# Optimization experiments

Measured on AMD Instinct MI355X. Metric: run time of the kernel, lower is better.

The kernel has to match this reference:

```python
import jax, jax.numpy as jnp
import numpy as np

B, T, H = 2048, 512, 128  # batch, seq_len, lstm_dim
IN = 1  # LSTMCell input dim = 1 + c_dim (condition=False)


def setup_inputs() -> dict:
    key = jax.random.key(0)
    ks = jax.random.split(key, 10)
    s_ih = 1.0 / np.sqrt(H)
    return {
        "x": jax.random.normal(ks[0], (B, T), dtype=jnp.float32),
        "hx0": jax.random.normal(ks[1], (B, H), dtype=jnp.float32),
        "cx0": jax.random.normal(ks[2], (B, H), dtype=jnp.float32),
        # PyTorch LSTMCell params, gate order (i, f, g, o)
        "W_ih": jax.random.uniform(ks[3], (4 * H, IN), jnp.float32, -s_ih, s_ih),
        "W_hh": jax.random.uniform(ks[4], (4 * H, H), jnp.float32, -s_ih, s_ih),
        "b_ih": jax.random.uniform(ks[5], (4 * H,), jnp.float32, -s_ih, s_ih),
        "b_hh": jax.random.uniform(ks[6], (4 * H,), jnp.float32, -s_ih, s_ih),
        # final Linear(lstm_dim, 1) + Sigmoid
        "W_mlp": jax.random.uniform(ks[7], (1, H), jnp.float32, -s_ih, s_ih),
        "b_mlp": jax.random.uniform(ks[8], (1,), jnp.float32, -s_ih, s_ih),
    }


def _lstm_forward(x, hx0, cx0, W_ih, W_hh, b_ih, b_hh):
    # Precompute input contribution for all steps: x is [B, T], input dim 1.
    # gates_x[t] = x[:, t:t+1] @ W_ih.T  -> [T, B, 4H]
    gates_x = x.T[:, :, None] * W_ih[:, 0][None, None, :] + (b_ih + b_hh)

    def step(carry, gx):
        hx, cx = carry
        gates = gx + hx @ W_hh.T  # [B, 4H]
        i, f, g, o = jnp.split(gates, 4, axis=-1)
        i = jax.nn.sigmoid(i)
        f = jax.nn.sigmoid(f)
        g = jnp.tanh(g)
        o = jax.nn.sigmoid(o)
        cx = f * cx + i * g
        hx = o * jnp.tanh(cx)
        return (hx, cx), None

    (hx, cx), _ = jax.lax.scan(step, (hx0, cx0), gates_x)
    return hx


def reference(x, hx0, cx0, W_ih, W_hh, b_ih, b_hh, W_mlp, b_mlp):
    hx = _lstm_forward(x, hx0, cx0, W_ih, W_hh, b_ih, b_hh)
    return jax.nn.sigmoid(hx @ W_mlp.T + b_mlp)  # [B, 1]
```

## Files before the change

### kernel.cpp

```cpp
#include <hip/hip_runtime.h>

#define Hdim 128
#define Tlen 512
#define BT 8
#define STR 136

typedef __attribute__((ext_vector_type(8))) _Float16 f16x8;
typedef __attribute__((ext_vector_type(2))) _Float16 f16x2;
typedef __attribute__((ext_vector_type(4))) float f32x4;

__device__ __forceinline__ f32x4 mfma_f16(f16x8 a, f16x8 b, f32x4 c) {
  return __builtin_amdgcn_mfma_f32_16x16x32_f16(a, b, c, 0, 0, 0);
}
__device__ __forceinline__ float dpp_shl8(float old, float v) {
  int r = __builtin_amdgcn_update_dpp(__builtin_bit_cast(int, old),
                                      __builtin_bit_cast(int, v),
                                      0x108 , 0xF, 0xF, false);
  return __builtin_bit_cast(float, r);
}

__global__ __launch_bounds__(512, 2)
void lstm_disc_kernel(const float* __restrict__ x, const float* __restrict__ hx0,
                      const float* __restrict__ cx0, const float* __restrict__ W_ih,
                      const float* __restrict__ W_hh, const float* __restrict__ b_ih,
                      const float* __restrict__ b_hh, const float* __restrict__ W_mlp,
                      const float* __restrict__ b_mlp, float* __restrict__ out) {
  __shared__ _Float16 hbuf0[BT * STR];
  __shared__ _Float16 hbuf1[BT * STR];

  const int tid  = threadIdx.x;
  const int w    = tid >> 6;
  const int lane = tid & 63;
  const int l16  = lane & 15;
  const int quad = lane >> 4;
  const int b0   = blockIdx.x * BT;
  const int bb   = l16 & 7;
  const bool hi  = (l16 < 8);
  const int uoff = quad * 4 + (hi ? 0 : 2);
  const int ub   = 16 * w + uoff;

  f16x8 wh[4][4];
  float wihG[4][2], biasG[4][2];
#pragma unroll
  for (int s = 0; s < 4; s++) {
    const float sc = (s == 2) ? 2.88539008f : -1.44269504f;
    const int j = 16 * w + 128 * s + l16;
#pragma unroll
    for (int q = 0; q < 4; q++) {
      const float* p = W_hh + j * Hdim + q * 32 + quad * 8;
      f16x8 f;
#pragma unroll
      for (int e = 0; e < 8; e++) f[e] = (_Float16)(p[e] * sc);
      wh[s][q] = f;
    }
#pragma unroll
    for (int r2 = 0; r2 < 2; r2++) {
      const int j2 = 16 * w + 128 * s + uoff + r2;
      wihG[s][r2]  = W_ih[j2] * sc;
      biasG[s][r2] = (b_ih[j2] + b_hh[j2]) * sc;
    }
  }

  for (int i = tid; i < BT * Hdim; i += 512) {
    const int b = i >> 7, k = i & 127;
    hbuf0[b * STR + k] = (_Float16)hx0[(b0 + b) * Hdim + k];
  }

  float c[2] = {cx0[(b0 + bb) * Hdim + ub], cx0[(b0 + bb) * Hdim + ub + 1]};

  const float* xp = x + (b0 + bb) * Tlen;
  float xv[4] = {xp[0], xp[1], xp[2], xp[3]};

  __syncthreads();

  const f32x4 Z = {0.0f, 0.0f, 0.0f, 0.0f};

  auto step = [&](const _Float16* __restrict__ src, _Float16* __restrict__ dst,
                  float xcur) {
    f16x8 bfrag[4];
#pragma unroll
    for (int q = 0; q < 4; q++)
      bfrag[q] = *(const f16x8*)&src[bb * STR + q * 32 + quad * 8];

    f32x4 a[4];
#pragma unroll
    for (int s = 0; s < 4; s++) a[s] = mfma_f16(wh[s][0], bfrag[0], Z);
#pragma unroll
    for (int q = 1; q < 4; q++)
#pragma unroll
      for (int s = 0; s < 4; s++) a[s] = mfma_f16(wh[s][q], bfrag[q], a[s]);

    float G[4][2];
#pragma unroll
    for (int s = 0; s < 4; s++)
#pragma unroll
      for (int r2 = 0; r2 < 2; r2++) {
        float g = dpp_shl8(a[s][r2], a[s][2 + r2]);
        G[s][r2] = __builtin_fmaf(xcur, wihG[s][r2], g + biasG[s][r2]);
      }

    float hv[2];
#pragma unroll
    for (int r2 = 0; r2 < 2; r2++) {
      float iv = __builtin_amdgcn_rcpf(1.0f + __builtin_amdgcn_exp2f(G[0][r2]));
      float fv = __builtin_amdgcn_rcpf(1.0f + __builtin_amdgcn_exp2f(G[1][r2]));
      float gv = 1.0f - 2.0f * __builtin_amdgcn_rcpf(
                              __builtin_amdgcn_exp2f(G[2][r2]) + 1.0f);
      float ov = __builtin_amdgcn_rcpf(1.0f + __builtin_amdgcn_exp2f(G[3][r2]));
      float cn = __builtin_fmaf(fv, c[r2], iv * gv);
      c[r2] = cn;
      float tc = 1.0f - 2.0f * __builtin_amdgcn_rcpf(
                              __builtin_amdgcn_exp2f(cn * 2.88539008f) + 1.0f);
      hv[r2] = ov * tc;
    }
    f16x2 hp;
    hp[0] = (_Float16)hv[0];
    hp[1] = (_Float16)hv[1];
    *(f16x2*)&dst[bb * STR + ub] = hp;

    __syncthreads();
  };

  for (int t = 0; t < Tlen; t += 4) {
    const int tn = t + 4;
    float xa = xp[(tn     < Tlen) ? tn     : Tlen - 1];
    float xb = xp[(tn + 1 < Tlen) ? tn + 1 : Tlen - 1];
    float xc = xp[(tn + 2 < Tlen) ? tn + 2 : Tlen - 1];
    float xd = xp[(tn + 3 < Tlen) ? tn + 3 : Tlen - 1];
    step(hbuf0, hbuf1, xv[0]);
    step(hbuf1, hbuf0, xv[1]);
    step(hbuf0, hbuf1, xv[2]);
    step(hbuf1, hbuf0, xv[3]);
    xv[0] = xa; xv[1] = xb; xv[2] = xc; xv[3] = xd;
  }

  if (tid < BT) {
    float s = 0.0f;
#pragma unroll 8
    for (int k = 0; k < Hdim; k++)
      s += (float)hbuf0[tid * STR + k] * W_mlp[k];
    out[b0 + tid] = __builtin_amdgcn_rcpf(
        1.0f + __builtin_amdgcn_exp2f((s + b_mlp[0]) * -1.44269504f));
  }
}

extern "C" void kernel_launch(void* const* d_in, const int* in_sizes, int n_in,
                              void* d_out, int out_size, void* d_ws, size_t ws_size,
                              hipStream_t stream) {
  const float* x     = (const float*)d_in[0];
  const float* hx0   = (const float*)d_in[1];
  const float* cx0   = (const float*)d_in[2];
  const float* W_ih  = (const float*)d_in[3];
  const float* W_hh  = (const float*)d_in[4];
  const float* b_ih  = (const float*)d_in[5];
  const float* b_hh  = (const float*)d_in[6];
  const float* W_mlp = (const float*)d_in[7];
  const float* b_mlp = (const float*)d_in[8];
  float* out = (float*)d_out;

  const int B = in_sizes[1] / Hdim;
  dim3 grid(B / BT), block(512);
  lstm_disc_kernel<<<grid, block, 0, stream>>>(x, hx0, cx0, W_ih, W_hh, b_ih,
                                               b_hh, W_mlp, b_mlp, out);
}
```

Measured before the change: 361.2 us.

## Split batch tile into two half-groups and overlap their MFMA with gate math

Splits the 8-row batch tile into two 4-row groups that alternate phases. Each phase runs the MFMA matrix product for one group while doing the gate nonlinearities and cell update for the other, hiding MFMA latency behind transcendental work. The DPP shuffle is replaced by lane selects, and each lane now owns one hidden unit per group. This doubles the number of barriers per timestep, and the MFMAs now run on half-populated batch columns.

```diff
diff --git a/kernel.cpp b/kernel.cpp
--- a/kernel.cpp
+++ b/kernel.cpp
@@ -6,17 +6,10 @@
 #define STR 136
 
 typedef __attribute__((ext_vector_type(8))) _Float16 f16x8;
-typedef __attribute__((ext_vector_type(2))) _Float16 f16x2;
 typedef __attribute__((ext_vector_type(4))) float f32x4;
 
 __device__ __forceinline__ f32x4 mfma_f16(f16x8 a, f16x8 b, f32x4 c) {
   return __builtin_amdgcn_mfma_f32_16x16x32_f16(a, b, c, 0, 0, 0);
-}
-__device__ __forceinline__ float dpp_shl8(float old, float v) {
-  int r = __builtin_amdgcn_update_dpp(__builtin_bit_cast(int, old),
-                                      __builtin_bit_cast(int, v),
-                                      0x108 , 0xF, 0xF, false);
-  return __builtin_bit_cast(float, r);
 }
 
 __global__ __launch_bounds__(512, 2)
@@ -34,13 +27,14 @@
   const int l16  = lane & 15;
   const int quad = lane >> 4;
   const int b0   = blockIdx.x * BT;
-  const int bb   = l16 & 7;
-  const bool hi  = (l16 < 8);
-  const int uoff = quad * 4 + (hi ? 0 : 2);
-  const int ub   = 16 * w + uoff;
+  const int bg   = l16 & 3;
+  const int uu   = quad * 4 + (l16 >> 2);
+  const int ua   = 16 * w + uu;
+  const bool j1  = (l16 & 4) != 0;
+  const bool j2  = (l16 & 8) != 0;
 
   f16x8 wh[4][4];
-  float wihG[4][2], biasG[4][2];
+  float wihG[4], biasG[4];
 #pragma unroll
   for (int s = 0; s < 4; s++) {
     const float sc = (s == 2) ? 2.88539008f : -1.44269504f;
@@ -53,12 +47,9 @@
       for (int e = 0; e < 8; e++) f[e] = (_Float16)(p[e] * sc);
       wh[s][q] = f;
     }
-#pragma unroll
-    for (int r2 = 0; r2 < 2; r2++) {
-      const int j2 = 16 * w + 128 * s + uoff + r2;
-      wihG[s][r2]  = W_ih[j2] * sc;
-      biasG[s][r2] = (b_ih[j2] + b_hh[j2]) * sc;
-    }
+    const int jr = 16 * w + 128 * s + uu;
+    wihG[s]  = W_ih[jr] * sc;
+    biasG[s] = (b_ih[jr] + b_hh[jr]) * sc;
   }
 
   for (int i = tid; i < BT * Hdim; i += 512) {
@@ -66,79 +57,87 @@
     hbuf0[b * STR + k] = (_Float16)hx0[(b0 + b) * Hdim + k];
   }
 
-  float c[2] = {cx0[(b0 + bb) * Hdim + ub], cx0[(b0 + bb) * Hdim + ub + 1]};
+  float cA = cx0[(b0 + bg) * Hdim + ua];
+  float cB = cx0[(b0 + 4 + bg) * Hdim + ua];
 
-  const float* xp = x + (b0 + bb) * Tlen;
-  float xv[4] = {xp[0], xp[1], xp[2], xp[3]};
+  const float* xpA = x + (b0 + bg) * Tlen;
+  const float* xpB = x + (b0 + 4 + bg) * Tlen;
+  float xA0 = xpA[0], xA1 = xpA[1], xB0 = xpB[0], xB1 = xpB[1];
 
   __syncthreads();
 
   const f32x4 Z = {0.0f, 0.0f, 0.0f, 0.0f};
+  f16x8 bfA[4], bfB[4];
+  f32x4 accA[4], accB[4];
 
-  auto step = [&](const _Float16* __restrict__ src, _Float16* __restrict__ dst,
-                  float xcur) {
-    f16x8 bfrag[4];
 #pragma unroll
-    for (int q = 0; q < 4; q++)
-      bfrag[q] = *(const f16x8*)&src[bb * STR + q * 32 + quad * 8];
+  for (int q = 0; q < 4; q++) {
+    bfA[q] = *(const f16x8*)&hbuf0[bg * STR + q * 32 + quad * 8];
+    bfB[q] = *(const f16x8*)&hbuf0[(4 + bg) * STR + q * 32 + quad * 8];
+  }
+#pragma unroll
+  for (int s = 0; s < 4; s++) accA[s] = mfma_f16(wh[s][0], bfA[0], Z);
+#pragma unroll
+  for (int q = 1; q < 4; q++)
+#pragma unroll
+    for (int s = 0; s < 4; s++) accA[s] = mfma_f16(wh[s][q], bfA[q], accA[s]);
+  __syncthreads();
 
-    f32x4 a[4];
+  auto phase = [&](f32x4 (&accX)[4], f16x8 (&bfX)[4],
+                   f32x4 (&accY)[4], f16x8 (&bfY)[4],
+                   float& cY, float xY, _Float16* __restrict__ bufY) {
+    float G[4];
 #pragma unroll
-    for (int s = 0; s < 4; s++) a[s] = mfma_f16(wh[s][0], bfrag[0], Z);
+    for (int s = 0; s < 4; s++) {
+      float t0 = j1 ? accY[s][1] : accY[s][0];
+      float t1 = j1 ? accY[s][3] : accY[s][2];
+      float g  = j2 ? t1 : t0;
+      G[s] = __builtin_fmaf(xY, wihG[s], g + biasG[s]);
+    }
+
+#pragma unroll
+    for (int s = 0; s < 4; s++) accX[s] = mfma_f16(wh[s][0], bfX[0], Z);
 #pragma unroll
     for (int q = 1; q < 4; q++)
 #pragma unroll
-      for (int s = 0; s < 4; s++) a[s] = mfma_f16(wh[s][q], bfrag[q], a[s]);
+      for (int s = 0; s < 4; s++) accX[s] = mfma_f16(wh[s][q], bfX[q], accX[s]);
 
-    float G[4][2];
-#pragma unroll
-    for (int s = 0; s < 4; s++)
-#pragma unroll
-      for (int r2 = 0; r2 < 2; r2++) {
-        float g = dpp_shl8(a[s][r2], a[s][2 + r2]);
-        G[s][r2] = __builtin_fmaf(xcur, wihG[s][r2], g + biasG[s][r2]);
-      }
-
-    float hv[2];
-#pragma unroll
-    for (int r2 = 0; r2 < 2; r2++) {
-      float iv = __builtin_amdgcn_rcpf(1.0f + __builtin_amdgcn_exp2f(G[0][r2]));
-      float fv = __builtin_amdgcn_rcpf(1.0f + __builtin_amdgcn_exp2f(G[1][r2]));
-      float gv = 1.0f - 2.0f * __builtin_amdgcn_rcpf(
-                              __builtin_amdgcn_exp2f(G[2][r2]) + 1.0f);
-      float ov = __builtin_amdgcn_rcpf(1.0f + __builtin_amdgcn_exp2f(G[3][r2]));
-      float cn = __builtin_fmaf(fv, c[r2], iv * gv);
-      c[r2] = cn;
-      float tc = 1.0f - 2.0f * __builtin_amdgcn_rcpf(
-                              __builtin_amdgcn_exp2f(cn * 2.88539008f) + 1.0f);
-      hv[r2] = ov * tc;
-    }
-    f16x2 hp;
-    hp[0] = (_Float16)hv[0];
-    hp[1] = (_Float16)hv[1];
-    *(f16x2*)&dst[bb * STR + ub] = hp;
+    float iv = __builtin_amdgcn_rcpf(1.0f + __builtin_amdgcn_exp2f(G[0]));
+    float fv = __builtin_amdgcn_rcpf(1.0f + __builtin_amdgcn_exp2f(G[1]));
+    float gv = 1.0f - 2.0f * __builtin_amdgcn_rcpf(
+                            __builtin_amdgcn_exp2f(G[2]) + 1.0f);
+    float ov = __builtin_amdgcn_rcpf(1.0f + __builtin_amdgcn_exp2f(G[3]));
+    float cn = __builtin_fmaf(fv, cY, iv * gv);
+    cY = cn;
+    float tc = 1.0f - 2.0f * __builtin_amdgcn_rcpf(
+                            __builtin_amdgcn_exp2f(cn * 2.88539008f) + 1.0f);
+    float hv = ov * tc;
+    bufY[bg * STR + ua] = (_Float16)hv;
 
     __syncthreads();
+#pragma unroll
+    for (int q = 0; q < 4; q++)
+      bfY[q] = *(const f16x8*)&bufY[bg * STR + q * 32 + quad * 8];
   };
 
-  for (int t = 0; t < Tlen; t += 4) {
-    const int tn = t + 4;
-    float xa = xp[(tn     < Tlen) ? tn     : Tlen - 1];
-    float xb = xp[(tn + 1 < Tlen) ? tn + 1 : Tlen - 1];
-    float xc = xp[(tn + 2 < Tlen) ? tn + 2 : Tlen - 1];
-    float xd = xp[(tn + 3 < Tlen) ? tn + 3 : Tlen - 1];
-    step(hbuf0, hbuf1, xv[0]);
-    step(hbuf1, hbuf0, xv[1]);
-    step(hbuf0, hbuf1, xv[2]);
-    step(hbuf1, hbuf0, xv[3]);
-    xv[0] = xa; xv[1] = xb; xv[2] = xc; xv[3] = xd;
+  for (int t = 0; t < Tlen; t += 2) {
+    const int tn = t + 2;
+    float nA0 = xpA[(tn     < Tlen) ? tn     : Tlen - 1];
+    float nA1 = xpA[(tn + 1 < Tlen) ? tn + 1 : Tlen - 1];
+    float nB0 = xpB[(tn     < Tlen) ? tn     : Tlen - 1];
+    float nB1 = xpB[(tn + 1 < Tlen) ? tn + 1 : Tlen - 1];
+    phase(accB, bfB, accA, bfA, cA, xA0, hbuf0);
+    phase(accA, bfA, accB, bfB, cB, xB0, hbuf0 + 4 * STR);
+    phase(accB, bfB, accA, bfA, cA, xA1, hbuf1);
+    phase(accA, bfA, accB, bfB, cB, xB1, hbuf1 + 4 * STR);
+    xA0 = nA0; xA1 = nA1; xB0 = nB0; xB1 = nB1;
   }
 
   if (tid < BT) {
     float s = 0.0f;
 #pragma unroll 8
     for (int k = 0; k < Hdim; k++)
-      s += (float)hbuf0[tid * STR + k] * W_mlp[k];
+      s += (float)hbuf1[tid * STR + k] * W_mlp[k];
     out[b0 + tid] = __builtin_amdgcn_rcpf(
         1.0f + __builtin_amdgcn_exp2f((s + b_mlp[0]) * -1.44269504f));
   }
```

After: 579.7 us. 1.6x slower.
